# Kernel tuning notes

Hardware: AMD Instinct MI355X
Metric: run time of the kernel (lower is better)

The kernel has to match this reference:

```python
import jax, jax.numpy as jnp
import numpy as np

B, S, D = 8, 1024, 1024          # batch, sentence_len, instance_size
H = 16                            # n_head
HEAD_SIZE = 1024                  # Head_size (== D here)
HD = HEAD_SIZE // H               # multi_head_size = 64


def setup_inputs() -> dict:
    key = jax.random.key(0)
    k1, k2, k3 = jax.random.split(key, 3)
    x = jax.random.normal(k1, (B, S, D), dtype=jnp.float32)
    padding_mask = jnp.ones((B, 1, S), dtype=jnp.float32)  # 1 = valid key token
    # nn.Linear(instance_size, 3*Head_size, bias=False): store as [D, 3*HEAD_SIZE]
    Wqkv = jax.random.normal(k2, (D, 3 * HEAD_SIZE), dtype=jnp.float32) / np.sqrt(D)
    # nn.Linear(Head_size, instance_size): weight [HEAD_SIZE, D] + bias [D]
    Wproj = jax.random.normal(k3, (HEAD_SIZE, D), dtype=jnp.float32) / np.sqrt(HEAD_SIZE)
    bproj = jnp.zeros((D,), dtype=jnp.float32)
    return {"x": x, "padding_mask": padding_mask, "Wqkv": Wqkv, "Wproj": Wproj, "bproj": bproj}


def reference(x, padding_mask, Wqkv, Wproj, bproj):
    Bn, Sn, _ = x.shape
    qkv = x @ Wqkv                                  # [B,S,3*HEAD_SIZE]
    q, k, v = jnp.split(qkv, 3, axis=2)
    # [B,S,H,hd] -> [B,H,S,hd]
    q = q.reshape(Bn, Sn, H, HD).transpose(0, 2, 1, 3)
    k = k.reshape(Bn, Sn, H, HD).transpose(0, 2, 1, 3)
    v = v.reshape(Bn, Sn, H, HD).transpose(0, 2, 1, 3)
    # scores [B,H,S,S]
    scores = jnp.einsum('bhqd,bhkd->bhqk', q, k) / np.sqrt(HD)
    # padding_mask [B,1,S] -> additive bias over key dim, broadcast over heads/queries
    mask_w = -(1.0 - padding_mask) * 1e10          # [B,1,S]
    scores = scores + mask_w[:, None]              # [B,1,1,S] broadcast
    probas = jax.nn.softmax(scores, axis=-1)
    probas = probas * padding_mask[:, None]        # zero out padded keys (as in torch code)
    # dropout p=0 (eval) -> identity
    out = jnp.einsum('bhqk,bhkd->bhqd', probas, v)  # [B,H,S,hd]
    out = out.transpose(0, 2, 1, 3).reshape(Bn, Sn, HEAD_SIZE)
    return out @ Wproj + bproj
```

## Files before the change

### kernel.cpp

```cpp
#include <hip/hip_runtime.h>
#include <stdint.h>

typedef short s16x8 __attribute__((ext_vector_type(8)));
typedef float f32x4 __attribute__((ext_vector_type(4)));
typedef unsigned short u16;
typedef unsigned short u16x4 __attribute__((ext_vector_type(4)));
typedef unsigned int u32x2 __attribute__((ext_vector_type(2)));

#define B_ 8
#define S_ 1024
#define C1 0.18033688f
#define KADV ((size_t)64 * 3072)

__device__ __forceinline__ u16 f2bf(float f) {
  union { float f; unsigned u; } v; v.f = f;
  unsigned u = v.u;
  unsigned r = (u + 0x7FFFu + ((u >> 16) & 1u)) >> 16;
  return (u16)r;
}

__device__ __forceinline__ void gll16(const u16* src, u16* dst) {
  __builtin_amdgcn_global_load_lds((const __attribute__((address_space(1))) void*)src,
                                   (__attribute__((address_space(3))) void*)dst, 16, 0, 0);
}

__global__ void k_cvt(const float* __restrict__ in, u16* __restrict__ out, int n4) {
  int i = blockIdx.x * blockDim.x + threadIdx.x;
  int stride = gridDim.x * blockDim.x;
  for (; i < n4; i += stride) {
    float4 v = ((const float4*)in)[i];
    u16x4 o;
    o.x = f2bf(v.x); o.y = f2bf(v.y); o.z = f2bf(v.z); o.w = f2bf(v.w);
    ((u16x4*)out)[i] = o;
  }
}

__global__ void k_mbias(const float* __restrict__ m, float* __restrict__ mb, int n) {
  int i = blockIdx.x * blockDim.x + threadIdx.x;
  if (i < n) mb[i] = (m[i] - 1.f) * 1.443e10f;
}

__global__ void k_tpose(const float* __restrict__ in, u16* __restrict__ out, int R, int C) {
  __shared__ float tile[64][65];
  int c0 = blockIdx.x * 64, r0 = blockIdx.y * 64;
  int t = threadIdx.x;
#pragma unroll
  for (int it = 0; it < 16; ++it) {
    int r = it * 4 + (t >> 6), c = t & 63;
    tile[r][c] = in[(size_t)(r0 + r) * C + c0 + c];
  }
  __syncthreads();
#pragma unroll
  for (int it = 0; it < 16; ++it) {
    int c = it * 4 + (t >> 6), r = t & 63;
    out[(size_t)(c0 + c) * R + r0 + r] = f2bf(tile[r][c]);
  }
}

template<int ROWS>
__device__ __forceinline__ void stage_swz(const u16* __restrict__ g, size_t goff, size_t ld,
                                          u16* lds, int wave, int lane) {
#pragma unroll
  for (int c = 0; c < ROWS / 32; ++c) {
    int jb = (wave * (ROWS / 32) + c) * 64;
    int j = jb + lane;
    int row = j >> 3;
    int s = (j & 7) ^ (row & 7);
    const u16* src = g + goff + (size_t)row * ld + s * 8;
    u16* dst = lds + jb * 8;
    gll16(src, dst);
  }
}

__device__ __forceinline__ s16x8 frag_read(const u16* lds, int row, int slotk) {
  int s = slotk ^ (row & 7);
  return *(const s16x8*)(lds + row * 64 + s * 8);
}

template<int BIAS, int OUT_F32, int QKV_VSPLIT>
__global__ __launch_bounds__(256, 2) void k_gemm(
    const u16* __restrict__ A, const u16* __restrict__ BT,
    void* __restrict__ Cout, const float* __restrict__ bias,
    int M, int N, int K) {
  __shared__ u16 sA[128 * 64];
  __shared__ u16 sB[128 * 64];
  int bid = blockIdx.x;
  int xcd = bid & 7, idx = bid >> 3;
  int tm = xcd * 8 + (idx & 7), tn = idx >> 3;
  int lane = threadIdx.x & 63, wave = threadIdx.x >> 6;
  int fr = lane & 15, g = lane >> 4;
  int wr = wave >> 1, wc = wave & 1;
  f32x4 acc[4][4] = {};
  for (int kt = 0; kt < (K >> 6); ++kt) {
    __syncthreads();
    stage_swz<128>(A, (size_t)(tm * 128) * K + kt * 64, K, sA, wave, lane);
    stage_swz<128>(BT, (size_t)(tn * 128) * K + kt * 64, K, sB, wave, lane);
    __syncthreads();
#pragma unroll
    for (int kk = 0; kk < 2; ++kk) {
      s16x8 af[4], bfr[4];
#pragma unroll
      for (int mi = 0; mi < 4; ++mi) af[mi] = frag_read(sA, wr * 64 + mi * 16 + fr, kk * 4 + g);
#pragma unroll
      for (int ni = 0; ni < 4; ++ni) bfr[ni] = frag_read(sB, wc * 64 + ni * 16 + fr, kk * 4 + g);
#pragma unroll
      for (int mi = 0; mi < 4; ++mi)
#pragma unroll
        for (int ni = 0; ni < 4; ++ni)
          acc[mi][ni] = __builtin_amdgcn_mfma_f32_16x16x32_bf16(af[mi], bfr[ni], acc[mi][ni], 0, 0, 0);
    }
  }
  if (QKV_VSPLIT && tn >= 16) {
#pragma unroll
    for (int mi = 0; mi < 4; ++mi) {
#pragma unroll
      for (int ni = 0; ni < 4; ++ni) {
        int row = tm * 128 + wr * 64 + mi * 16 + g * 4;
        int col = tn * 128 + wc * 64 + ni * 16 + fr;
        int colV = col - 2048;
        int rp = ((row >> 10) * 16 + (colV >> 6)) * 64 + (colV & 63);
        u16x4 o4;
#pragma unroll
        for (int r = 0; r < 4; ++r) o4[r] = f2bf(acc[mi][ni][r]);
        *(u16x4*)((u16*)Cout + (size_t)rp * 3072 + 2048 + (row & 1023)) = o4;
      }
    }
    return;
  }
#pragma unroll
  for (int mi = 0; mi < 4; ++mi) {
#pragma unroll
    for (int ni = 0; ni < 4; ++ni) {
      int row = tm * 128 + wr * 64 + mi * 16 + g * 4;
      int col = tn * 128 + wc * 64 + ni * 16 + fr;
      float bv = BIAS ? bias[col] : 0.f;
#pragma unroll
      for (int r = 0; r < 4; ++r) {
        float v = acc[mi][ni][r] + bv;
        if (OUT_F32) ((float*)Cout)[(size_t)(row + r) * N + col] = v;
        else ((u16*)Cout)[(size_t)(row + r) * N + col] = f2bf(v);
      }
    }
  }
}

__global__ __launch_bounds__(256, 4) void k_attn(
    const u16* __restrict__ qkv, const float* __restrict__ mbias, u16* __restrict__ outb) {
  __shared__ u16 kls[2][64 * 64];
  __shared__ u16 vls[2][64 * 64];
  int bid = blockIdx.x;
  int wg = (bid & 7) * 128 + (bid >> 3);
  int qt = wg & 7, h = (wg >> 3) & 15, b = wg >> 7;
  int lane = threadIdx.x & 63, wave = threadIdx.x >> 6;
  int fr = lane & 15, g = lane >> 4;

  const size_t baseK = (size_t)(b * S_) * 3072 + 1024 + h * 64;
  const size_t baseV = (size_t)((b * 16 + h) * 64) * 3072 + 2048;
  const float* mbc = mbias + b * S_ + g * 4;

  const size_t rowQA = (size_t)(b * S_ + qt * 128 + wave * 32 + fr) * 3072 + h * 64;
  const size_t rowQB = rowQA + (size_t)16 * 3072;
  s16x8 qfA0 = *(const s16x8*)(qkv + rowQA + g * 8);
  s16x8 qfA1 = *(const s16x8*)(qkv + rowQA + 32 + g * 8);
  s16x8 qfB0 = *(const s16x8*)(qkv + rowQB + g * 8);
  s16x8 qfB1 = *(const s16x8*)(qkv + rowQB + 32 + g * 8);

  int j0 = wave * 128 + lane, j1 = j0 + 64;
  int r0 = j0 >> 3, s0 = (j0 & 7) ^ (r0 & 7);
  int r1 = j1 >> 3, s1 = (j1 & 7) ^ (r1 & 7);
  const u16* kp0 = qkv + baseK + (size_t)r0 * 3072 + s0 * 8;
  const u16* kp1 = qkv + baseK + (size_t)r1 * 3072 + s1 * 8;
  const u16* vp0 = qkv + baseV + (size_t)r0 * 3072 + s0 * 8;
  const u16* vp1 = qkv + baseV + (size_t)r1 * 3072 + s1 * 8;
  u16* kd0 = (u16*)kls[0] + wave * 1024;
  u16* kd1 = kd0 + 512;
  u16* vd0 = (u16*)vls[0] + wave * 1024;
  u16* vd1 = vd0 + 512;

  const u16* kb = (const u16*)kls[0] + fr * 64;
  const u16* vb = (const u16*)vls[0] + fr * 64;
  const int sl0 = (g ^ (fr & 7)) * 8;
  const int sl4 = ((4 + g) ^ (fr & 7)) * 8;

  float seA = 0.f, seB = 0.f;
  f32x4 oaccA[4] = {};
  f32x4 oaccB[4] = {};

  gll16(kp0, kd0); gll16(kp1, kd1); gll16(vp0, vd0); gll16(vp1, vd1);
  kp0 += KADV; kp1 += KADV; vp0 += 64; vp1 += 64;

#define CHUNK_BODY(BUF)                                                          \
  do {                                                                           \
    f32x4 b40 = *(const f32x4*)(mbc);                                            \
    f32x4 b41 = *(const f32x4*)(mbc + 16);                                       \
    f32x4 b42 = *(const f32x4*)(mbc + 32);                                       \
    f32x4 b43 = *(const f32x4*)(mbc + 48);                                       \
    unsigned wvA[4][2], wvB[4][2];                                               \
    float sA0 = 0.f, sA1 = 0.f, sA2 = 0.f, sA3 = 0.f;                            \
    float sB0 = 0.f, sB1 = 0.f, sB2 = 0.f, sB3 = 0.f;                            \
    _Pragma("unroll") for (int kt = 0; kt < 4; ++kt) {                           \
      s16x8 kf0 = *(const s16x8*)(kb + (BUF)*4096 + kt * 1024 + sl0);            \
      s16x8 kf1 = *(const s16x8*)(kb + (BUF)*4096 + kt * 1024 + sl4);            \
      f32x4 sa = {0.f, 0.f, 0.f, 0.f}, sb = {0.f, 0.f, 0.f, 0.f};                \
      sa = __builtin_amdgcn_mfma_f32_16x16x32_bf16(kf0, qfA0, sa, 0, 0, 0);      \
      sa = __builtin_amdgcn_mfma_f32_16x16x32_bf16(kf1, qfA1, sa, 0, 0, 0);      \
      sb = __builtin_amdgcn_mfma_f32_16x16x32_bf16(kf0, qfB0, sb, 0, 0, 0);      \
      sb = __builtin_amdgcn_mfma_f32_16x16x32_bf16(kf1, qfB1, sb, 0, 0, 0);      \
      f32x4 b4 = (kt == 0) ? b40 : (kt == 1) ? b41 : (kt == 2) ? b42 : b43;      \
      float eA0 = __builtin_amdgcn_exp2f(fmaf(sa[0], C1, b4[0]));                \
      float eA1 = __builtin_amdgcn_exp2f(fmaf(sa[1], C1, b4[1]));                \
      float eA2 = __builtin_amdgcn_exp2f(fmaf(sa[2], C1, b4[2]));                \
      float eA3 = __builtin_amdgcn_exp2f(fmaf(sa[3], C1, b4[3]));                \
      float eB0 = __builtin_amdgcn_exp2f(fmaf(sb[0], C1, b4[0]));                \
      float eB1 = __builtin_amdgcn_exp2f(fmaf(sb[1], C1, b4[1]));                \
      float eB2 = __builtin_amdgcn_exp2f(fmaf(sb[2], C1, b4[2]));                \
      float eB3 = __builtin_amdgcn_exp2f(fmaf(sb[3], C1, b4[3]));                \
      sA0 += eA0; sA1 += eA1; sA2 += eA2; sA3 += eA3;                            \
      sB0 += eB0; sB1 += eB1; sB2 += eB2; sB3 += eB3;                            \
      asm("v_cvt_pk_bf16_f32 %0, %1, %2" : "=v"(wvA[kt][0]) : "v"(eA0), "v"(eA1)); \
      asm("v_cvt_pk_bf16_f32 %0, %1, %2" : "=v"(wvA[kt][1]) : "v"(eA2), "v"(eA3)); \
      asm("v_cvt_pk_bf16_f32 %0, %1, %2" : "=v"(wvB[kt][0]) : "v"(eB0), "v"(eB1)); \
      asm("v_cvt_pk_bf16_f32 %0, %1, %2" : "=v"(wvB[kt][1]) : "v"(eB2), "v"(eB3)); \
    }                                                                            \
    seA += (sA0 + sA1) + (sA2 + sA3);                                            \
    seB += (sB0 + sB1) + (sB2 + sB3);                                            \
    _Pragma("unroll") for (int kc = 0; kc < 2; ++kc) {                           \
      unsigned xa0 = wvA[2 * kc][0], ya0 = wvA[2 * kc + 1][0];                   \
      unsigned xa1 = wvA[2 * kc][1], ya1 = wvA[2 * kc + 1][1];                   \
      unsigned xb0 = wvB[2 * kc][0], yb0 = wvB[2 * kc + 1][0];                   \
      unsigned xb1 = wvB[2 * kc][1], yb1 = wvB[2 * kc + 1][1];                   \
      asm("v_permlane32_swap_b32 %0, %1" : "+v"(xa0), "+v"(ya0));                \
      asm("v_permlane16_swap_b32 %0, %1" : "+v"(xa0), "+v"(ya0));                \
      asm("v_permlane32_swap_b32 %0, %1" : "+v"(xa1), "+v"(ya1));                \
      asm("v_permlane16_swap_b32 %0, %1" : "+v"(xa1), "+v"(ya1));                \
      asm("v_permlane32_swap_b32 %0, %1" : "+v"(xb0), "+v"(yb0));                \
      asm("v_permlane16_swap_b32 %0, %1" : "+v"(xb0), "+v"(yb0));                \
      asm("v_permlane32_swap_b32 %0, %1" : "+v"(xb1), "+v"(yb1));                \
      asm("v_permlane16_swap_b32 %0, %1" : "+v"(xb1), "+v"(yb1));                \
      union { unsigned u[4]; s16x8 v; } pfa, pfb;                                \
      pfa.u[0] = xa0; pfa.u[1] = xa1; pfa.u[2] = ya0; pfa.u[3] = ya1;            \
      pfb.u[0] = xb0; pfb.u[1] = xb1; pfb.u[2] = yb0; pfb.u[3] = yb1;            \
      _Pragma("unroll") for (int dbi = 0; dbi < 4; ++dbi) {                      \
        s16x8 vf = *(const s16x8*)(vb + (BUF)*4096 + dbi * 1024 +                \
                                   ((kc) ? sl4 : sl0));                          \
        oaccA[dbi] = __builtin_amdgcn_mfma_f32_16x16x32_bf16(vf, pfa.v,          \
                                                             oaccA[dbi], 0, 0, 0); \
        oaccB[dbi] = __builtin_amdgcn_mfma_f32_16x16x32_bf16(vf, pfb.v,          \
                                                             oaccB[dbi], 0, 0, 0); \
      }                                                                          \
    }                                                                            \
    mbc += 64;                                                                   \
  } while (0)

#pragma unroll 1
  for (int chp = 0; chp < 8; ++chp) {
    __syncthreads();
    gll16(kp0, kd0 + 4096); gll16(kp1, kd1 + 4096);
    gll16(vp0, vd0 + 4096); gll16(vp1, vd1 + 4096);
    kp0 += KADV; kp1 += KADV; vp0 += 64; vp1 += 64;
    CHUNK_BODY(0);
    __syncthreads();
    if (chp < 7) {
      gll16(kp0, kd0); gll16(kp1, kd1); gll16(vp0, vd0); gll16(vp1, vd1);
      kp0 += KADV; kp1 += KADV; vp0 += 64; vp1 += 64;
    }
    CHUNK_BODY(1);
  }
#undef CHUNK_BODY

  seA += __shfl_xor(seA, 16);
  seA += __shfl_xor(seA, 32);
  seB += __shfl_xor(seB, 16);
  seB += __shfl_xor(seB, 32);
  float invA = 1.f / seA, invB = 1.f / seB;
  u16* orowA = outb + (size_t)(b * S_ + qt * 128 + wave * 32 + fr) * 1024 + h * 64;
  u16* orowB = orowA + (size_t)16 * 1024;
#pragma unroll
  for (int dbi = 0; dbi < 4; ++dbi) {
    float a0 = oaccA[dbi][0] * invA, a1 = oaccA[dbi][1] * invA;
    float a2 = oaccA[dbi][2] * invA, a3 = oaccA[dbi][3] * invA;
    float b0 = oaccB[dbi][0] * invB, b1 = oaccB[dbi][1] * invB;
    float b2 = oaccB[dbi][2] * invB, b3 = oaccB[dbi][3] * invB;
    unsigned wa0, wa1, wb0, wb1;
    asm("v_cvt_pk_bf16_f32 %0, %1, %2" : "=v"(wa0) : "v"(a0), "v"(a1));
    asm("v_cvt_pk_bf16_f32 %0, %1, %2" : "=v"(wa1) : "v"(a2), "v"(a3));
    asm("v_cvt_pk_bf16_f32 %0, %1, %2" : "=v"(wb0) : "v"(b0), "v"(b1));
    asm("v_cvt_pk_bf16_f32 %0, %1, %2" : "=v"(wb1) : "v"(b2), "v"(b3));
    u32x2 wwa = {wa0, wa1}, wwb = {wb0, wb1};
    *(u32x2*)(orowA + dbi * 16 + g * 4) = wwa;
    *(u32x2*)(orowB + dbi * 16 + g * 4) = wwb;
  }
}

extern "C" void kernel_launch(void* const* d_in, const int* in_sizes, int n_in,
                              void* d_out, int out_size, void* d_ws, size_t ws_size,
                              hipStream_t stream) {
  const float* x     = (const float*)d_in[0];
  const float* pmask = (const float*)d_in[1];
  const float* Wqkv  = (const float*)d_in[2];
  const float* Wproj = (const float*)d_in[3];
  const float* bproj = (const float*)d_in[4];

  u16* xB      = (u16*)d_ws;
  u16* WqkvT   = xB + (size_t)8192 * 1024;
  u16* WprojT  = WqkvT + (size_t)3072 * 1024;
  u16* qkv     = WprojT + (size_t)1024 * 1024;
  u16* attn    = qkv + (size_t)8192 * 3072;
  float* mbias = (float*)(attn + (size_t)8192 * 1024);

  k_cvt<<<2048, 256, 0, stream>>>(x, xB, 8192 * 1024 / 4);
  k_mbias<<<32, 256, 0, stream>>>(pmask, mbias, 8192);
  k_tpose<<<dim3(3072 / 64, 1024 / 64), 256, 0, stream>>>(Wqkv, WqkvT, 1024, 3072);
  k_tpose<<<dim3(1024 / 64, 1024 / 64), 256, 0, stream>>>(Wproj, WprojT, 1024, 1024);
  k_gemm<0, 0, 1><<<64 * 24, 256, 0, stream>>>(xB, WqkvT, (void*)qkv, (const float*)nullptr, 8192, 3072, 1024);
  k_attn<<<1024, 256, 0, stream>>>(qkv, mbias, attn);
  k_gemm<1, 1, 0><<<64 * 8, 256, 0, stream>>>(attn, WprojT, d_out, bproj, 8192, 1024, 1024);
}
```

Measured before the change: 153.1 us.

## Double-buffer GEMM LDS with 256x128 tiles, 8 waves, and interleaved prefetch

Rewrites the bf16 GEMM kernel to use 256x128 output tiles with 512 threads and double-buffered LDS. The next K-slice is fetched with global_load_lds while the MFMAs run, split into A and B halves between two compute phases, and s_setprio raises priority during the MFMA bursts. The aim is to hide global load latency, which the old single-buffer loop with two syncthreads per step exposed, and to reuse each B tile across more rows. In exchange, LDS use per block grows to 96KB, which may limit occupancy, and correctness now depends on the hand-placed barriers and waitcnts.

```diff
diff --git a/kernel.cpp b/kernel.cpp
--- a/kernel.cpp
+++ b/kernel.cpp
@@ -57,66 +57,113 @@
   }
 }
 
-template<int ROWS>
-__device__ __forceinline__ void stage_swz(const u16* __restrict__ g, size_t goff, size_t ld,
-                                          u16* lds, int wave, int lane) {
-#pragma unroll
-  for (int c = 0; c < ROWS / 32; ++c) {
-    int jb = (wave * (ROWS / 32) + c) * 64;
-    int j = jb + lane;
-    int row = j >> 3;
-    int s = (j & 7) ^ (row & 7);
-    const u16* src = g + goff + (size_t)row * ld + s * 8;
-    u16* dst = lds + jb * 8;
-    gll16(src, dst);
-  }
-}
-
-__device__ __forceinline__ s16x8 frag_read(const u16* lds, int row, int slotk) {
-  int s = slotk ^ (row & 7);
-  return *(const s16x8*)(lds + row * 64 + s * 8);
-}
-
 template<int BIAS, int OUT_F32, int QKV_VSPLIT>
-__global__ __launch_bounds__(256, 2) void k_gemm(
+__global__ __launch_bounds__(512, 2) void k_gemm(
     const u16* __restrict__ A, const u16* __restrict__ BT,
     void* __restrict__ Cout, const float* __restrict__ bias,
     int M, int N, int K) {
-  __shared__ u16 sA[128 * 64];
-  __shared__ u16 sB[128 * 64];
+  __shared__ u16 lds[2 * 24576];
   int bid = blockIdx.x;
   int xcd = bid & 7, idx = bid >> 3;
-  int tm = xcd * 8 + (idx & 7), tn = idx >> 3;
-  int lane = threadIdx.x & 63, wave = threadIdx.x >> 6;
+  int mtx = (M >> 8) >> 3;
+  int tm = xcd * mtx + (idx % mtx), tn = idx / mtx;
+  int tid = threadIdx.x;
+  int lane = tid & 63, wave = tid >> 6;
   int fr = lane & 15, g = lane >> 4;
-  int wr = wave >> 1, wc = wave & 1;
+  int wm = wave >> 1, wn = wave & 1;
+  const int sl0 = (g ^ (fr & 7)) * 8;
+  const int sl4 = ((4 + g) ^ (fr & 7)) * 8;
+
+  const u16* pA[4];
+  const u16* pB[2];
+#pragma unroll
+  for (int c = 0; c < 4; ++c) {
+    int j = c * 512 + tid, row = j >> 3, s = (j & 7) ^ (row & 7);
+    pA[c] = A + (size_t)(tm * 256 + row) * K + s * 8;
+  }
+#pragma unroll
+  for (int c = 0; c < 2; ++c) {
+    int j = c * 512 + tid, row = j >> 3, s = (j & 7) ^ (row & 7);
+    pB[c] = BT + (size_t)(tn * 128 + row) * K + s * 8;
+  }
+  const int dstw = wave * 512;
+  const int aOff = (wm * 64 + fr) * 64;
+  const int bOff = 16384 + (wn * 64 + fr) * 64;
+
   f32x4 acc[4][4] = {};
-  for (int kt = 0; kt < (K >> 6); ++kt) {
-    __syncthreads();
-    stage_swz<128>(A, (size_t)(tm * 128) * K + kt * 64, K, sA, wave, lane);
-    stage_swz<128>(BT, (size_t)(tn * 128) * K + kt * 64, K, sB, wave, lane);
-    __syncthreads();
-#pragma unroll
-    for (int kk = 0; kk < 2; ++kk) {
-      s16x8 af[4], bfr[4];
-#pragma unroll
-      for (int mi = 0; mi < 4; ++mi) af[mi] = frag_read(sA, wr * 64 + mi * 16 + fr, kk * 4 + g);
-#pragma unroll
-      for (int ni = 0; ni < 4; ++ni) bfr[ni] = frag_read(sB, wc * 64 + ni * 16 + fr, kk * 4 + g);
-#pragma unroll
-      for (int mi = 0; mi < 4; ++mi)
-#pragma unroll
-        for (int ni = 0; ni < 4; ++ni)
-          acc[mi][ni] = __builtin_amdgcn_mfma_f32_16x16x32_bf16(af[mi], bfr[ni], acc[mi][ni], 0, 0, 0);
-    }
-  }
+  int nt = K >> 6;
+
+#pragma unroll
+  for (int c = 0; c < 4; ++c) { gll16(pA[c], lds + c * 4096 + dstw); pA[c] += 64; }
+#pragma unroll
+  for (int c = 0; c < 2; ++c) { gll16(pB[c], lds + 16384 + c * 4096 + dstw); pB[c] += 64; }
+  asm volatile("s_waitcnt vmcnt(0)" ::: "memory");
+  asm volatile("s_barrier" ::: "memory");
+
+#pragma unroll 1
+  for (int t = 0; t < nt; ++t) {
+    const u16* rb = lds + (t & 1) * 24576;
+    u16* sb = lds + ((t & 1) ^ 1) * 24576 + dstw;
+    s16x8 bf[4][2], af[2][2];
+#pragma unroll
+    for (int ni = 0; ni < 4; ++ni) {
+      bf[ni][0] = *(const s16x8*)(rb + bOff + ni * 1024 + sl0);
+      bf[ni][1] = *(const s16x8*)(rb + bOff + ni * 1024 + sl4);
+    }
+#pragma unroll
+    for (int mi = 0; mi < 2; ++mi) {
+      af[mi][0] = *(const s16x8*)(rb + aOff + mi * 1024 + sl0);
+      af[mi][1] = *(const s16x8*)(rb + aOff + mi * 1024 + sl4);
+    }
+    if (t < nt - 1) {
+#pragma unroll
+      for (int c = 0; c < 4; ++c) { gll16(pA[c], sb + c * 4096); pA[c] += 64; }
+    }
+    asm volatile("s_barrier" ::: "memory");
+    asm volatile("s_waitcnt lgkmcnt(0)" ::: "memory");
+    __builtin_amdgcn_sched_barrier(0);
+    __builtin_amdgcn_s_setprio(1);
+#pragma unroll
+    for (int mi = 0; mi < 2; ++mi)
+#pragma unroll
+      for (int ni = 0; ni < 4; ++ni) {
+        acc[mi][ni] = __builtin_amdgcn_mfma_f32_16x16x32_bf16(af[mi][0], bf[ni][0], acc[mi][ni], 0, 0, 0);
+        acc[mi][ni] = __builtin_amdgcn_mfma_f32_16x16x32_bf16(af[mi][1], bf[ni][1], acc[mi][ni], 0, 0, 0);
+      }
+    __builtin_amdgcn_s_setprio(0);
+    asm volatile("s_barrier" ::: "memory");
+#pragma unroll
+    for (int mi = 0; mi < 2; ++mi) {
+      af[mi][0] = *(const s16x8*)(rb + aOff + (mi + 2) * 1024 + sl0);
+      af[mi][1] = *(const s16x8*)(rb + aOff + (mi + 2) * 1024 + sl4);
+    }
+    if (t < nt - 1) {
+#pragma unroll
+      for (int c = 0; c < 2; ++c) { gll16(pB[c], sb + 16384 + c * 4096); pB[c] += 64; }
+    }
+    asm volatile("s_barrier" ::: "memory");
+    asm volatile("s_waitcnt lgkmcnt(0)" ::: "memory");
+    __builtin_amdgcn_sched_barrier(0);
+    __builtin_amdgcn_s_setprio(1);
+#pragma unroll
+    for (int mi = 0; mi < 2; ++mi)
+#pragma unroll
+      for (int ni = 0; ni < 4; ++ni) {
+        acc[mi + 2][ni] = __builtin_amdgcn_mfma_f32_16x16x32_bf16(af[mi][0], bf[ni][0], acc[mi + 2][ni], 0, 0, 0);
+        acc[mi + 2][ni] = __builtin_amdgcn_mfma_f32_16x16x32_bf16(af[mi][1], bf[ni][1], acc[mi + 2][ni], 0, 0, 0);
+      }
+    __builtin_amdgcn_s_setprio(0);
+    if (t < nt - 1) asm volatile("s_waitcnt vmcnt(0)" ::: "memory");
+    asm volatile("s_barrier" ::: "memory");
+  }
+
   if (QKV_VSPLIT && tn >= 16) {
 #pragma unroll
     for (int mi = 0; mi < 4; ++mi) {
 #pragma unroll
       for (int ni = 0; ni < 4; ++ni) {
-        int row = tm * 128 + wr * 64 + mi * 16 + g * 4;
-        int col = tn * 128 + wc * 64 + ni * 16 + fr;
+        int row = tm * 256 + wm * 64 + mi * 16 + g * 4;
+        int col = tn * 128 + wn * 64 + ni * 16 + fr;
         int colV = col - 2048;
         int rp = ((row >> 10) * 16 + (colV >> 6)) * 64 + (colV & 63);
         u16x4 o4;
@@ -131,8 +178,8 @@
   for (int mi = 0; mi < 4; ++mi) {
 #pragma unroll
     for (int ni = 0; ni < 4; ++ni) {
-      int row = tm * 128 + wr * 64 + mi * 16 + g * 4;
-      int col = tn * 128 + wc * 64 + ni * 16 + fr;
+      int row = tm * 256 + wm * 64 + mi * 16 + g * 4;
+      int col = tn * 128 + wn * 64 + ni * 16 + fr;
       float bv = BIAS ? bias[col] : 0.f;
 #pragma unroll
       for (int r = 0; r < 4; ++r) {
@@ -312,7 +359,7 @@
   k_mbias<<<32, 256, 0, stream>>>(pmask, mbias, 8192);
   k_tpose<<<dim3(3072 / 64, 1024 / 64), 256, 0, stream>>>(Wqkv, WqkvT, 1024, 3072);
   k_tpose<<<dim3(1024 / 64, 1024 / 64), 256, 0, stream>>>(Wproj, WprojT, 1024, 1024);
-  k_gemm<0, 0, 1><<<64 * 24, 256, 0, stream>>>(xB, WqkvT, (void*)qkv, (const float*)nullptr, 8192, 3072, 1024);
+  k_gemm<0, 0, 1><<<768, 512, 0, stream>>>(xB, WqkvT, (void*)qkv, (const float*)nullptr, 8192, 3072, 1024);
   k_attn<<<1024, 256, 0, stream>>>(qkv, mbias, attn);
-  k_gemm<1, 1, 0><<<64 * 8, 256, 0, stream>>>(attn, WprojT, d_out, bproj, 8192, 1024, 1024);
-}
+  k_gemm<1, 1, 0><<<256, 512, 0, stream>>>(attn, WprojT, d_out, bproj, 8192, 1024, 1024);
+}
```

Measured after the change: 157.3 us. 1.03x slower.
